# Optimization experiments

Measured on AMD Instinct MI355X. Metric: run time of the kernel, lower is better.

Reference implementation:

```python
import jax, jax.numpy as jnp
import numpy as np

D_MODEL = 2048
N_HEADS = 16
N_KV_HEADS = 4
D_HEAD = 128
MAX_SEQ_LEN = 4096
RANK = 32
GAMMA_INIT = 0.05
ROPE_BASE = 10000.0


def setup_inputs() -> dict:
    key = jax.random.key(0)
    ks = jax.random.split(key, 10)
    B, T = 1, 2048
    s = lambda fan_in: 1.0 / np.sqrt(fan_in)
    x = jax.random.normal(ks[0], (B, T, D_MODEL), dtype=jnp.float32)
    Wq = jax.random.normal(ks[1], (D_MODEL, N_HEADS * D_HEAD), dtype=jnp.float32) * s(D_MODEL)
    Wk = jax.random.normal(ks[2], (D_MODEL, N_KV_HEADS * D_HEAD), dtype=jnp.float32) * s(D_MODEL)
    Wv = jax.random.normal(ks[3], (D_MODEL, N_KV_HEADS * D_HEAD), dtype=jnp.float32) * s(D_MODEL)
    Wo = jax.random.normal(ks[4], (N_HEADS * D_HEAD, D_MODEL), dtype=jnp.float32) * s(N_HEADS * D_HEAD)
    pol_dir = jax.random.normal(ks[5], (N_HEADS,), dtype=jnp.float32) * 0.1
    pol_WA = jax.random.normal(ks[6], (D_MODEL, RANK), dtype=jnp.float32) * s(D_MODEL)
    pol_WB = jax.random.normal(ks[7], (D_MODEL, RANK), dtype=jnp.float32) * s(D_MODEL)
    pol_gate = jnp.full((N_HEADS,), -3.0, dtype=jnp.float32)
    # gtp_gamma initialized so softplus(gtp_gamma) == geometric ALiBi-style gamma schedule
    slopes = np.linspace(3.0, -3.0, N_HEADS)
    gamma_t = np.clip(GAMMA_INIT * 2.0 ** slopes, 1e-4, None)
    gtp_gamma = jnp.asarray(np.log(np.expm1(gamma_t)), dtype=jnp.float32)
    return {"x": x, "Wq": Wq, "Wk": Wk, "Wv": Wv, "Wo": Wo,
            "pol_dir": pol_dir, "pol_WA": pol_WA, "pol_WB": pol_WB,
            "pol_gate": pol_gate, "gtp_gamma": gtp_gamma}


def _rope(x, offset=0):
    # x: [B,H,T,D]; standard rotate-half RoPE
    B, H, T, D = x.shape
    inv_freq = 1.0 / (ROPE_BASE ** (jnp.arange(0, D, 2, dtype=jnp.float32) / D))
    pos = jnp.arange(T, dtype=jnp.float32) + offset
    ang = pos[:, None] * inv_freq[None, :]          # [T, D/2]
    cos = jnp.cos(ang)[None, None]                  # [1,1,T,D/2]
    sin = jnp.sin(ang)[None, None]
    x1, x2 = x[..., : D // 2], x[..., D // 2 :]
    return jnp.concatenate([x1 * cos - x2 * sin, x2 * cos + x1 * sin], axis=-1)


def reference(x, Wq, Wk, Wv, Wo, pol_dir, pol_WA, pol_WB, pol_gate, gtp_gamma):
    B, T, _ = x.shape
    H, Hkv, D = N_HEADS, N_KV_HEADS, D_HEAD
    n_rep = H // Hkv
    Q = (x @ Wq).reshape(B, T, H, D).transpose(0, 2, 1, 3)     # [B,H,T,D]
    K = (x @ Wk).reshape(B, T, Hkv, D).transpose(0, 2, 1, 3)   # [B,Hkv,T,D]
    V = (x @ Wv).reshape(B, T, Hkv, D).transpose(0, 2, 1, 3)
    Q = _rope(Q)
    K = _rope(K)
    K = jnp.repeat(K, n_rep, axis=1)                           # [B,H,T,D]
    V = jnp.repeat(V, n_rep, axis=1)

    # ---- attention bias ----
    idx = jnp.arange(T)
    delta = (idx[:, None] - idx[None, :]).astype(jnp.float32)  # [T,T], i - j
    causal = delta >= 0
    pol = jnp.clip(pol_dir, -1.0, 1.0)
    polarity_bias = -pol[:, None, None] * (delta / float(MAX_SEQ_LEN))[None]     # [H,T,T]
    gamma = jnp.maximum(jax.nn.softplus(gtp_gamma), 1e-6)
    gtp_bias = -gamma[:, None, None] * jnp.maximum(delta, 0.0)[None]             # [H,T,T]
    bias = (polarity_bias + gtp_bias)[None]                                      # [1,H,T,T]
    # low-rank content-dependent sigmoid bilinear term (prefill: q_len == k_len)
    A = x @ pol_WA                                                               # [B,T,r]
    Bm = x @ pol_WB                                                              # [B,T,r]
    M = jax.nn.sigmoid(jnp.einsum('bir,bjr->bij', A, Bm))                        # [B,T,T]
    gate = jax.nn.sigmoid(pol_gate)[None, :, None, None]
    bias = bias + gate * M[:, None]                                              # [B,H,T,T]
    neg_inf = jnp.finfo(bias.dtype).min
    bias = jnp.where(causal[None, None], bias, neg_inf)

    # ---- SDPA ----
    scores = jnp.einsum('bhid,bhjd->bhij', Q, K) / jnp.sqrt(jnp.float32(D)) + bias
    attn = jax.nn.softmax(scores, axis=-1)
    out = jnp.einsum('bhij,bhjd->bhid', attn, V)                                 # [B,H,T,D]
    out = out.transpose(0, 2, 1, 3).reshape(B, T, H * D)
    return out @ Wo
```

## Files before the change

### kernel.cpp

```cpp
#include <hip/hip_runtime.h>
#include <math.h>

typedef short bf16x8 __attribute__((ext_vector_type(8)));
typedef float f32x4  __attribute__((ext_vector_type(4)));

#define MFMA16 __builtin_amdgcn_mfma_f32_16x16x32_bf16
#define LOG2E 1.4426950408889634f

static __device__ __forceinline__ short f2bf(float f) {
  union { float f; unsigned u; } x; x.f = f;
  unsigned r = (x.u + 0x7FFFu + ((x.u >> 16) & 1u)) >> 16;
  return (short)r;
}
static __device__ __forceinline__ unsigned packbf(float a, float b) {
  return (unsigned)(unsigned short)f2bf(a) | ((unsigned)(unsigned short)f2bf(b) << 16);
}
static __device__ __forceinline__ float bf2f(short s) {
  union { unsigned u; float f; } x; x.u = ((unsigned)(unsigned short)s) << 16;
  return x.f;
}
static __device__ __forceinline__ void gload_lds16(const void* g, void* l) {
  __builtin_amdgcn_global_load_lds((const __attribute__((address_space(1))) void*)g,
                                   (__attribute__((address_space(3))) void*)l, 16, 0, 0);
}
static __device__ __forceinline__ float ex2(float x) {
  float r; asm("v_exp_f32 %0, %1" : "=v"(r) : "v"(x)); return r;
}
static __device__ __forceinline__ float rcpf(float x) {
  float r; asm("v_rcp_f32 %0, %1" : "=v"(r) : "v"(x)); return r;
}
static __device__ __forceinline__ unsigned cvtpk(float lo, float hi) {
  unsigned r; asm("v_cvt_pk_bf16_f32 %0, %1, %2" : "=v"(r) : "v"(lo), "v"(hi));
  return r;
}

__device__ __forceinline__ void tr_tile(
    const float* __restrict__ in, short* __restrict__ out,
    int K, int N, int nt, int kt, float (*t)[33])
{
  int n0 = nt * 32, k0 = kt * 32;
  int tx = threadIdx.x & 31, ty = threadIdx.x >> 5;
  #pragma unroll
  for (int i = 0; i < 4; ++i)
    t[ty + 8 * i][tx] = in[(size_t)(k0 + ty + 8 * i) * N + n0 + tx];
  __syncthreads();
  #pragma unroll
  for (int i = 0; i < 4; ++i)
    out[(size_t)(n0 + ty + 8 * i) * K + k0 + tx] = f2bf(t[tx][ty + 8 * i]);
}

__global__ __launch_bounds__(256) void prep_kernel(
    const float* __restrict__ x, const float* __restrict__ Wq,
    const float* __restrict__ Wk, const float* __restrict__ Wv,
    const float* __restrict__ WA, const float* __restrict__ WB,
    short* __restrict__ xb, short* __restrict__ Wqt, short* __restrict__ Wkt,
    short* __restrict__ Wvt, short* __restrict__ WABt)
{
  __shared__ float t[32][33];
  int b = blockIdx.x;
  if (b < 4096)       tr_tile(Wq, Wqt, 2048, 2048, b & 63, b >> 6, t);
  else if (b < 5120)  { int c = b - 4096; tr_tile(Wk, Wkt, 2048, 512, c & 15, c >> 4, t); }
  else if (b < 6144)  { int c = b - 5120; tr_tile(Wv, Wvt, 2048, 512, c & 15, c >> 4, t); }
  else if (b < 6208)  { int c = b - 6144; tr_tile(WA, WABt, 2048, 32, 0, c, t); }
  else if (b < 6272)  { int c = b - 6208; tr_tile(WB, WABt + 32 * 2048, 2048, 32, 0, c, t); }
  else {
    int i = (b - 6272) * 256 + threadIdx.x;
    float4 v = ((const float4*)x)[i];
    short4 o; o.x = f2bf(v.x); o.y = f2bf(v.y); o.z = f2bf(v.z); o.w = f2bf(v.w);
    ((short4*)xb)[i] = o;
  }
}

__global__ __launch_bounds__(256) void mid_kernel(
    const float* __restrict__ Wo, short* __restrict__ Wot,
    short* __restrict__ Q, short* __restrict__ K)
{
  __shared__ float t[32][33];
  int b = blockIdx.x;
  if (b < 4096) { tr_tile(Wo, Wot, 2048, 2048, b & 63, b >> 6, t); return; }
  int idx = (b - 4096) * 256 + threadIdx.x;
  int d  = idx & 63;
  int hh = (idx >> 6) % 20;
  int tt = idx / (20 * 64);
  short* base = (hh < 16) ? Q + (size_t)tt * 2048 + hh * 128 + d
                          : K + (size_t)tt * 512 + (hh - 16) * 128 + d;
  float inv = __expf((float)d * -0.14391156831212789f);
  float ang = (float)tt * inv;
  float sn, cs;
  __sincosf(ang, &sn, &cs);
  float x1 = bf2f(base[0]), x2 = bf2f(base[64]);
  base[0]  = f2bf(x1 * cs - x2 * sn);
  base[64] = f2bf(x2 * cs + x1 * sn);
}

__device__ __forceinline__ void gemm12864_core(
    const short* __restrict__ A, const short* __restrict__ Bt,
    int m0, int n0, int Kd, short* Asm , short* Bsm ,
    f32x4 acc[4][2])
{
  const int tid = threadIdx.x;
  const int lane = tid & 63, w = tid >> 6;
  const int lr = lane & 15, g4 = lane >> 4;
  const int wm = w >> 1, wn = w & 1;

  for (int k0 = 0; k0 < Kd; k0 += 64) {
    #pragma unroll
    for (int s = 0; s < 4; ++s) {
      int c = (s * 4 + w) * 64 + lane;
      int row = c >> 3, q = c & 7;
      gload_lds16(A + (size_t)(m0 + row) * Kd + k0 + (q ^ (row & 7)) * 8,
                  Asm + c * 8);
    }
    #pragma unroll
    for (int s = 0; s < 2; ++s) {
      int c = (s * 4 + w) * 64 + lane;
      int row = c >> 3, q = c & 7;
      gload_lds16(Bt + (size_t)(n0 + row) * Kd + k0 + (q ^ (row & 7)) * 8,
                  Bsm + c * 8);
    }
    __syncthreads();
    #pragma unroll
    for (int kk = 0; kk < 2; ++kk) {
      bf16x8 af[4], bff[2];
      #pragma unroll
      for (int mi = 0; mi < 4; ++mi) {
        int row = wm * 64 + mi * 16 + lr;
        af[mi] = *(const bf16x8*)(Asm + row * 64 +
                                  ((kk * 4 + g4) ^ (lr & 7)) * 8);
      }
      #pragma unroll
      for (int ni = 0; ni < 2; ++ni) {
        int row = wn * 32 + ni * 16 + lr;
        bff[ni] = *(const bf16x8*)(Bsm + row * 64 +
                                   ((kk * 4 + g4) ^ (lr & 7)) * 8);
      }
      #pragma unroll
      for (int mi = 0; mi < 4; ++mi)
        #pragma unroll
        for (int ni = 0; ni < 2; ++ni)
          acc[mi][ni] = MFMA16(af[mi], bff[ni], acc[mi][ni], 0, 0, 0);
    }
    __syncthreads();
  }
}

__global__ __launch_bounds__(256, 3) void gemm_qkv_kernel(
    const short* __restrict__ xb, const short* __restrict__ Wqt,
    const short* __restrict__ Wkt, const short* __restrict__ Wvt,
    const short* __restrict__ WABt,
    short* __restrict__ Qb, short* __restrict__ Kb, short* __restrict__ Vtb,
    short* __restrict__ Ab, short* __restrict__ Bb)
{
  __shared__ __align__(16) short Asm[128 * 64];
  __shared__ __align__(16) short Bsm[64 * 64];
  f32x4 acc[4][2];
  #pragma unroll
  for (int i = 0; i < 4; ++i)
    #pragma unroll
    for (int j = 0; j < 2; ++j) acc[i][j] = (f32x4){0.f, 0.f, 0.f, 0.f};

  const int bid = (int)blockIdx.x;
  const int swz = (bid & 7) * 98 + (bid >> 3);
  const int bx = swz % 49, by = swz / 49;

  const short* Bt; int mode, nl0;
  if (bx < 32)      { Bt = Wqt;  nl0 = bx * 64;        mode = 0; }
  else if (bx < 40) { Bt = Wkt;  nl0 = (bx - 32) * 64; mode = 1; }
  else if (bx < 48) { Bt = Wvt;  nl0 = (bx - 40) * 64; mode = 2; }
  else              { Bt = WABt; nl0 = 0;              mode = 3; }

  gemm12864_core(xb, Bt, by * 128, nl0, 2048, Asm, Bsm, acc);

  const int tid = threadIdx.x, lane = tid & 63, w = tid >> 6;
  const int lr = lane & 15, g4 = lane >> 4, wm = w >> 1, wn = w & 1;
  #pragma unroll
  for (int mi = 0; mi < 4; ++mi) {
    #pragma unroll
    for (int ni = 0; ni < 2; ++ni) {
      int mb = by * 128 + wm * 64 + mi * 16 + g4 * 4;
      int ncl = wn * 32 + ni * 16 + lr;
      int nc = nl0 + ncl;
      if (mode == 0) {
        #pragma unroll
        for (int r = 0; r < 4; ++r)
          Qb[(size_t)(mb + r) * 2048 + nc] = f2bf(acc[mi][ni][r]);
      } else if (mode == 1) {
        #pragma unroll
        for (int r = 0; r < 4; ++r)
          Kb[(size_t)(mb + r) * 512 + nc] = f2bf(acc[mi][ni][r]);
      } else if (mode == 2) {
        uint2 uu;
        uu.x = packbf(acc[mi][ni][0], acc[mi][ni][1]);
        uu.y = packbf(acc[mi][ni][2], acc[mi][ni][3]);
        *(uint2*)(Vtb + (size_t)nc * 2048 + mb) = uu;
      } else {
        #pragma unroll
        for (int r = 0; r < 4; ++r) {
          float sv = acc[mi][ni][r];
          if (ncl < 32) Ab[(size_t)(mb + r) * 32 + ncl] = f2bf(sv * LOG2E);
          else          Bb[(size_t)(mb + r) * 32 + (ncl - 32)] = f2bf(sv);
        }
      }
    }
  }
}

__global__ __launch_bounds__(256, 3) void gemm_out_kernel(
    const short* __restrict__ AO, const short* __restrict__ Wot,
    float* __restrict__ out)
{
  __shared__ __align__(16) short Asm[128 * 64];
  __shared__ __align__(16) short Bsm[64 * 64];
  f32x4 acc[4][2];
  #pragma unroll
  for (int i = 0; i < 4; ++i)
    #pragma unroll
    for (int j = 0; j < 2; ++j) acc[i][j] = (f32x4){0.f, 0.f, 0.f, 0.f};

  const int bid = (int)blockIdx.x;
  const int swz = (bid & 7) * 64 + (bid >> 3);
  const int bx = swz % 32, by = swz / 32;

  gemm12864_core(AO, Wot, by * 128, bx * 64, 2048, Asm, Bsm, acc);

  const int tid = threadIdx.x, lane = tid & 63, w = tid >> 6;
  const int lr = lane & 15, g4 = lane >> 4, wm = w >> 1, wn = w & 1;
  #pragma unroll
  for (int mi = 0; mi < 4; ++mi)
    #pragma unroll
    for (int ni = 0; ni < 2; ++ni) {
      int mb = by * 128 + wm * 64 + mi * 16 + g4 * 4;
      int nc = bx * 64 + wn * 32 + ni * 16 + lr;
      #pragma unroll
      for (int r = 0; r < 4; ++r)
        out[(size_t)(mb + r) * 2048 + nc] = acc[mi][ni][r];
    }
}

__global__ __launch_bounds__(256, 2) void attn_kernel(
    const short* __restrict__ Qg, const short* __restrict__ Kg,
    const short* __restrict__ Vtg, const short* __restrict__ Ag,
    const short* __restrict__ Bg, const float* __restrict__ pol_dir,
    const float* __restrict__ pol_gate, const float* __restrict__ gtp_gamma,
    short* __restrict__ AO)
{
  __shared__ __align__(16) char lds[73728];
  char* const K0s = lds;
  char* const K1s = lds + 16384;
  char* const V0s = lds + 32768;
  char* const V1s = lds + 49152;
  char* const Pb  = lds + 65536;

  const int tid = threadIdx.x;
  const int lane = tid & 63, w = tid >> 6;
  const int lr = lane & 15, g4 = lane >> 4;
  const int h  = blockIdx.x;
  const int by = blockIdx.y;
  const int qt = (by < 16) ? (31 - by) : (by - 16);
  const int q0 = qt * 64;
  const int kvh = h >> 2;
  const short* Kh = Kg + kvh * 128;
  const short* Vh = Vtg + (size_t)(kvh * 128) * 2048;

  float pol   = fminf(fmaxf(pol_dir[h], -1.f), 1.f);
  float gamma = fmaxf(log1pf(__expf(gtp_gamma[h])), 1e-6f);
  float gate  = (1.f / (1.f + __expf(-pol_gate[h]))) * LOG2E;
  const float c_h  = -(pol * (1.f / 4096.f) + gamma) * LOG2E;
  const float c16  = 16.f * c_h;
  const float chr1 = c_h, chr2 = c_h + c_h, chr3 = chr2 + c_h;
  const float sc = 0.08838834764831845f * LOG2E;
  const f32x4 z4 = {0.f, 0.f, 0.f, 0.f};

  #pragma unroll
  for (int s = 0; s < 4; ++s) {
    int idx = (w * 4 + s) * 64 + lane;
    int row = idx >> 4, slot = idx & 15;
    gload_lds16(Kh + (size_t)row * 512 + (slot ^ (row & 7)) * 8,
                K0s + (w * 4 + s) * 1024);
  }
  #pragma unroll
  for (int s = 0; s < 4; ++s) {
    int idx = (w * 4 + s) * 64 + lane;
    int row = idx >> 3, slot = idx & 7;
    gload_lds16(Vh + (size_t)row * 2048 + (slot ^ (row & 7)) * 8,
                V0s + (w * 4 + s) * 1024);
  }
  bf16x8 bA0, bA1, bA2, bA3, bB0, bB1, bB2, bB3;
  bA0 = *(const bf16x8*)(Bg + (size_t)(0 * 16 + lr) * 32 + g4 * 8);
  bA1 = *(const bf16x8*)(Bg + (size_t)(1 * 16 + lr) * 32 + g4 * 8);
  bA2 = *(const bf16x8*)(Bg + (size_t)(2 * 16 + lr) * 32 + g4 * 8);
  bA3 = *(const bf16x8*)(Bg + (size_t)(3 * 16 + lr) * 32 + g4 * 8);

  #pragma unroll
  for (int s = 0; s < 4; ++s) {
    int c = tid + s * 256;
    int row = c >> 4, sl = c & 15;
    int4 v = *(const int4*)(Qg + (size_t)(q0 + row) * 2048 + h * 128 + sl * 8);
    *(int4*)(K1s + row * 256 + ((sl * 16) ^ ((row & 7) << 4))) = v;
  }
  {
    int row = tid >> 2, sl = tid & 3;
    int4 va = *(const int4*)(Ag + (size_t)(q0 + row) * 32 + sl * 8);
    *(int4*)(Pb + row * 80 + sl * 16) = va;
  }
  asm volatile("s_waitcnt lgkmcnt(0)" ::: "memory");
  __builtin_amdgcn_s_barrier();

  bf16x8 qf[4];
  #pragma unroll
  for (int kk = 0; kk < 4; ++kk)
    qf[kk] = *(const bf16x8*)(K1s + (w * 16 + lr) * 256 +
                              ((kk * 64 + g4 * 16) ^ ((lr & 7) << 4)));
  bf16x8 afr = *(const bf16x8*)(Pb + (w * 16 + lr) * 80 + g4 * 16);
  asm volatile("s_waitcnt lgkmcnt(0)" ::: "memory");
  __builtin_amdgcn_s_barrier();

  f32x4 acc_o[8];
  #pragma unroll
  for (int i = 0; i < 8; ++i) acc_o[i] = z4;
  float m_st = -INFINITY, l_st = 0.f;
  char* const Pw = Pb + w * 2048;

#define ATTN_TILE(JT, KC, VC, KN, VN, BC0, BC1, BC2, BC3, BN0, BN1, BN2, BN3) \
  do {                                                                        \
    const int j0 = (JT) * 64;                                                 \
    const bool pf = (JT) < qt;                                                \
    if (pf) {                                                                 \
      _Pragma("unroll")                                                       \
      for (int s = 0; s < 4; ++s) {                                           \
        int idx = (w * 4 + s) * 64 + lane;                                    \
        int row = idx >> 4, slot = idx & 15;                                  \
        gload_lds16(Kh + (size_t)(j0 + 64 + row) * 512 + (slot ^ (row & 7)) * 8, \
                    (KN) + (w * 4 + s) * 1024);                               \
      }                                                                       \
      _Pragma("unroll")                                                       \
      for (int s = 0; s < 4; ++s) {                                           \
        int idx = (w * 4 + s) * 64 + lane;                                    \
        int row = idx >> 3, slot = idx & 7;                                   \
        gload_lds16(Vh + (size_t)row * 2048 + (j0 + 64) + (slot ^ (row & 7)) * 8, \
                    (VN) + (w * 4 + s) * 1024);                               \
      }                                                                       \
      BN0 = *(const bf16x8*)(Bg + (size_t)(j0 + 64 + 0 * 16 + lr) * 32 + g4 * 8); \
      BN1 = *(const bf16x8*)(Bg + (size_t)(j0 + 64 + 1 * 16 + lr) * 32 + g4 * 8); \
      BN2 = *(const bf16x8*)(Bg + (size_t)(j0 + 64 + 2 * 16 + lr) * 32 + g4 * 8); \
      BN3 = *(const bf16x8*)(Bg + (size_t)(j0 + 64 + 3 * 16 + lr) * 32 + g4 * 8); \
      asm volatile("s_waitcnt vmcnt(12)" ::: "memory");                       \
    } else {                                                                  \
      asm volatile("s_waitcnt vmcnt(0)" ::: "memory");                        \
    }                                                                         \
    __builtin_amdgcn_s_barrier();         \
    f32x4 acc_s[4], md4[4];                                                   \
    __builtin_amdgcn_s_setprio(1);                                            \
    _Pragma("unroll")                                                         \
    for (int cb = 0; cb < 4; ++cb) {                                          \
      acc_s[cb] = z4;                                                         \
      _Pragma("unroll")                                                       \
      for (int kk = 0; kk < 4; ++kk) {                                        \
        bf16x8 kf = *(const bf16x8*)((KC) + (cb * 16 + lr) * 256 +            \
                                     ((kk * 64 + g4 * 16) ^ ((lr & 7) << 4)));\
        acc_s[cb] = MFMA16(kf, qf[kk], acc_s[cb], 0, 0, 0);                   \
      }                                                                       \
    }                                                                         \
    md4[0] = MFMA16(BC0, afr, z4, 0, 0, 0);                                   \
    md4[1] = MFMA16(BC1, afr, z4, 0, 0, 0);                                   \
    md4[2] = MFMA16(BC2, afr, z4, 0, 0, 0);                                   \
    md4[3] = MFMA16(BC3, afr, z4, 0, 0, 0);                                   \
    __builtin_amdgcn_s_setprio(0);                                            \
    const int dq = q0 + w * 16 + lr - j0;                                     \
    float bq = c_h * (float)(dq - g4 * 4);                                    \
    _Pragma("unroll")                                                         \
    for (int cb = 0; cb < 4; ++cb) {                                          \
      float bcb = bq - c16 * (float)cb;                                       \
      float sig0 = rcpf(1.f + ex2(-md4[cb][0]));                              \
      float sig1 = rcpf(1.f + ex2(-md4[cb][1]));                              \
      float sig2 = rcpf(1.f + ex2(-md4[cb][2]));                              \
      float sig3 = rcpf(1.f + ex2(-md4[cb][3]));                              \
      acc_s[cb][0] = fmaf(acc_s[cb][0], sc, fmaf(gate, sig0, bcb));           \
      acc_s[cb][1] = fmaf(acc_s[cb][1], sc, fmaf(gate, sig1, bcb - chr1));    \
      acc_s[cb][2] = fmaf(acc_s[cb][2], sc, fmaf(gate, sig2, bcb - chr2));    \
      acc_s[cb][3] = fmaf(acc_s[cb][3], sc, fmaf(gate, sig3, bcb - chr3));    \
    }                                                                         \
    if ((JT) == qt) {                                                         \
      _Pragma("unroll")                                                       \
      for (int cb = 0; cb < 4; ++cb)                                          \
        _Pragma("unroll")                                                     \
        for (int r = 0; r < 4; ++r)                                           \
          if (cb * 16 + g4 * 4 + r > dq) acc_s[cb][r] = -INFINITY;            \
    }                                                                         \
    float t0 = fmaxf(fmaxf(acc_s[0][0], acc_s[0][1]), acc_s[0][2]);           \
    float t1 = fmaxf(fmaxf(acc_s[0][3], acc_s[1][0]), acc_s[1][1]);           \
    float t2 = fmaxf(fmaxf(acc_s[1][2], acc_s[1][3]), acc_s[2][0]);           \
    float t3 = fmaxf(fmaxf(acc_s[2][1], acc_s[2][2]), acc_s[2][3]);           \
    float t4 = fmaxf(fmaxf(acc_s[3][0], acc_s[3][1]), acc_s[3][2]);           \
    float mx = fmaxf(fmaxf(fmaxf(t0, t1), t2),                                \
                     fmaxf(fmaxf(t3, t4), acc_s[3][3]));                      \
    mx = fmaxf(mx, __shfl_xor(mx, 16));                                       \
    mx = fmaxf(mx, __shfl_xor(mx, 32));                                       \
    if (!__all(mx - m_st <= 11.5415603f)) {                                   \
      float mn = fmaxf(m_st, mx);                                             \
      float es = ex2(m_st - mn);                                              \
      l_st *= es;                                                             \
      m_st = mn;                                                              \
      float es4[4];                                                           \
      _Pragma("unroll")                                                       \
      for (int r = 0; r < 4; ++r) es4[r] = __shfl(es, g4 * 4 + r, 64);        \
      _Pragma("unroll")                                                       \
      for (int db = 0; db < 8; ++db)                                          \
        _Pragma("unroll")                                                     \
        for (int r = 0; r < 4; ++r) acc_o[db][r] *= es4[r];                   \
    }                                                                         \
    float rs = 0.f;                                                           \
    _Pragma("unroll")                                                         \
    for (int cb = 0; cb < 4; ++cb)                                            \
      _Pragma("unroll")                                                       \
      for (int r = 0; r < 4; ++r) {                                           \
        float p = ex2(acc_s[cb][r] - m_st);                                   \
        acc_s[cb][r] = p;                                                     \
        rs += p;                                                              \
      }                                                                       \
    rs += __shfl_xor(rs, 16);                                                 \
    rs += __shfl_xor(rs, 32);                                                 \
    l_st += rs;                                                               \
    _Pragma("unroll")                                                         \
    for (int cb = 0; cb < 4; ++cb) {                                          \
      uint2 uu;                                                               \
      uu.x = cvtpk(acc_s[cb][0], acc_s[cb][1]);                               \
      uu.y = cvtpk(acc_s[cb][2], acc_s[cb][3]);                               \
      *(uint2*)(Pw + lr * 128 + ((cb * 32 + g4 * 8) ^ ((lr & 7) << 4))) = uu; \
    }                                                                         \
    asm volatile("s_waitcnt lgkmcnt(0)" ::: "memory");                        \
    __builtin_amdgcn_sched_barrier(0);                                        \
    __builtin_amdgcn_s_setprio(1);                                            \
    _Pragma("unroll")                                                         \
    for (int kk = 0; kk < 2; ++kk) {                                          \
      bf16x8 pfr = *(const bf16x8*)(Pw + lr * 128 +                           \
                                    ((kk * 64 + g4 * 16) ^ ((lr & 7) << 4))); \
      _Pragma("unroll")                                                       \
      for (int db = 0; db < 8; ++db) {                                        \
        bf16x8 vf = *(const bf16x8*)((VC) + (db * 16 + lr) * 128 +            \
                                     ((kk * 64 + g4 * 16) ^ ((lr & 7) << 4)));\
        acc_o[db] = MFMA16(pfr, vf, acc_o[db], 0, 0, 0);                      \
      }                                                                       \
    }                                                                         \
    __builtin_amdgcn_s_setprio(0);                                            \
    asm volatile("s_waitcnt lgkmcnt(0)" ::: "memory");                        \
    __builtin_amdgcn_s_barrier();           \
  } while (0)

  for (int jt = 0; jt <= qt; jt += 2) {
    ATTN_TILE(jt, K0s, V0s, K1s, V1s, bA0, bA1, bA2, bA3, bB0, bB1, bB2, bB3);
    if (jt + 1 <= qt)
      ATTN_TILE(jt + 1, K1s, V1s, K0s, V0s, bB0, bB1, bB2, bB3,
                bA0, bA1, bA2, bA3);
  }
#undef ATTN_TILE

  float lrcp[4];
  #pragma unroll
  for (int r = 0; r < 4; ++r) lrcp[r] = 1.f / __shfl(l_st, g4 * 4 + r, 64);
  #pragma unroll
  for (int db = 0; db < 8; ++db)
    #pragma unroll
    for (int r = 0; r < 4; ++r)
      AO[(size_t)(q0 + w * 16 + g4 * 4 + r) * 2048 + h * 128 + db * 16 + lr] =
          f2bf(acc_o[db][r] * lrcp[r]);
}

extern "C" void kernel_launch(void* const* d_in, const int* in_sizes, int n_in,
                              void* d_out, int out_size, void* d_ws, size_t ws_size,
                              hipStream_t stream) {
  const float* x         = (const float*)d_in[0];
  const float* Wq        = (const float*)d_in[1];
  const float* Wk        = (const float*)d_in[2];
  const float* Wv        = (const float*)d_in[3];
  const float* Wo        = (const float*)d_in[4];
  const float* pol_dir   = (const float*)d_in[5];
  const float* pol_WA    = (const float*)d_in[6];
  const float* pol_WB    = (const float*)d_in[7];
  const float* pol_gate  = (const float*)d_in[8];
  const float* gtp_gamma = (const float*)d_in[9];
  float* out = (float*)d_out;

  char* ws = (char*)d_ws;
  short* Qb   = (short*)(ws);
  short* Kb   = (short*)(ws + 8388608);
  short* Vtb  = (short*)(ws + 10485760);
  short* Ab   = (short*)(ws + 12582912);
  short* Bb   = (short*)(ws + 12713984);
  short* xb   = (short*)(ws + 12845056);
  short* Wot  = xb;
  short* Wqt  = (short*)(ws + 21233664);
  short* AO   = Wqt;
  short* Wkt  = (short*)(ws + 29622272);
  short* Wvt  = (short*)(ws + 31719424);
  short* WABt = (short*)(ws + 33816576);

  prep_kernel<<<10368, 256, 0, stream>>>(x, Wq, Wk, Wv, pol_WA, pol_WB,
                                         xb, Wqt, Wkt, Wvt, WABt);
  gemm_qkv_kernel<<<784, 256, 0, stream>>>(xb, Wqt, Wkt, Wvt, WABt,
                                           Qb, Kb, Vtb, Ab, Bb);
  mid_kernel<<<14336, 256, 0, stream>>>(Wo, Wot, Qb, Kb);
  attn_kernel<<<dim3(16, 32), 256, 0, stream>>>(Qb, Kb, Vtb, Ab, Bb,
                                                pol_dir, pol_gate, gtp_gamma, AO);
  gemm_out_kernel<<<512, 256, 0, stream>>>(AO, Wot, out);
}
```

Baseline: 156.9 us.

## Split long causal query tiles across two blocks and fold RoPE into attention

Query tiles 16-31 are each split into two KV ranges handled by separate blocks. The blocks write unnormalized bf16 partial outputs plus max/sum stats, and a new combine kernel merges them, which evens out the causal load imbalance. RoPE for Q is now applied inside the attention kernel from a precomputed cos/sin table, and only K gets a small standalone RoPE kernel. The Wo transpose moves into the prep kernel, and attention drops to a single V buffer (49KB LDS instead of 72KB) with the V and B-factor prefetch rescheduled. The costs are an extra launch, extra partial-output traffic, and bf16 rounding of the partials before the combine.

```diff
diff --git a/kernel.cpp b/kernel.cpp
--- a/kernel.cpp
+++ b/kernel.cpp
@@ -53,8 +53,10 @@
     const float* __restrict__ x, const float* __restrict__ Wq,
     const float* __restrict__ Wk, const float* __restrict__ Wv,
     const float* __restrict__ WA, const float* __restrict__ WB,
+    const float* __restrict__ Wo,
     short* __restrict__ xb, short* __restrict__ Wqt, short* __restrict__ Wkt,
-    short* __restrict__ Wvt, short* __restrict__ WABt)
+    short* __restrict__ Wvt, short* __restrict__ WABt, short* __restrict__ Wot,
+    float* __restrict__ RTab)
 {
   __shared__ float t[32][33];
   int b = blockIdx.x;
@@ -63,31 +65,36 @@
   else if (b < 6144)  { int c = b - 5120; tr_tile(Wv, Wvt, 2048, 512, c & 15, c >> 4, t); }
   else if (b < 6208)  { int c = b - 6144; tr_tile(WA, WABt, 2048, 32, 0, c, t); }
   else if (b < 6272)  { int c = b - 6208; tr_tile(WB, WABt + 32 * 2048, 2048, 32, 0, c, t); }
-  else {
+  else if (b < 10368) {
     int i = (b - 6272) * 256 + threadIdx.x;
     float4 v = ((const float4*)x)[i];
     short4 o; o.x = f2bf(v.x); o.y = f2bf(v.y); o.z = f2bf(v.z); o.w = f2bf(v.w);
     ((short4*)xb)[i] = o;
-  }
-}
-
-__global__ __launch_bounds__(256) void mid_kernel(
-    const float* __restrict__ Wo, short* __restrict__ Wot,
-    short* __restrict__ Q, short* __restrict__ K)
-{
-  __shared__ float t[32][33];
-  int b = blockIdx.x;
-  if (b < 4096) { tr_tile(Wo, Wot, 2048, 2048, b & 63, b >> 6, t); return; }
-  int idx = (b - 4096) * 256 + threadIdx.x;
+  } else if (b < 14464) {
+    int c = b - 10368;
+    tr_tile(Wo, Wot, 2048, 2048, c & 63, c >> 6, t);
+  } else {
+    int i = (b - 14464) * 256 + threadIdx.x;
+    int d = i & 63, tt = i >> 6;
+    float inv = __expf((float)d * -0.14391156831212789f);
+    float ang = (float)tt * inv;
+    float sn, cs;
+    __sincosf(ang, &sn, &cs);
+    RTab[(size_t)i * 2]     = cs;
+    RTab[(size_t)i * 2 + 1] = sn;
+  }
+}
+
+__global__ __launch_bounds__(256) void ropek_kernel(short* __restrict__ K,
+                                                    const float* __restrict__ RTab)
+{
+  int idx = blockIdx.x * 256 + threadIdx.x;
   int d  = idx & 63;
-  int hh = (idx >> 6) % 20;
-  int tt = idx / (20 * 64);
-  short* base = (hh < 16) ? Q + (size_t)tt * 2048 + hh * 128 + d
-                          : K + (size_t)tt * 512 + (hh - 16) * 128 + d;
-  float inv = __expf((float)d * -0.14391156831212789f);
-  float ang = (float)tt * inv;
-  float sn, cs;
-  __sincosf(ang, &sn, &cs);
+  int hh = (idx >> 6) & 3;
+  int tt = idx >> 8;
+  short* base = K + (size_t)tt * 512 + hh * 128 + d;
+  float cs = RTab[((size_t)tt * 64 + d) * 2];
+  float sn = RTab[((size_t)tt * 64 + d) * 2 + 1];
   float x1 = bf2f(base[0]), x2 = bf2f(base[64]);
   base[0]  = f2bf(x1 * cs - x2 * sn);
   base[64] = f2bf(x2 * cs + x1 * sn);
@@ -242,21 +249,23 @@
     const short* __restrict__ Vtg, const short* __restrict__ Ag,
     const short* __restrict__ Bg, const float* __restrict__ pol_dir,
     const float* __restrict__ pol_gate, const float* __restrict__ gtp_gamma,
-    short* __restrict__ AO)
-{
-  __shared__ __align__(16) char lds[73728];
+    const float* __restrict__ RTab, short* __restrict__ AO,
+    short* __restrict__ Opart, float* __restrict__ MLp)
+{
+  __shared__ __align__(16) char lds[49152];
   char* const K0s = lds;
   char* const K1s = lds + 16384;
-  char* const V0s = lds + 32768;
-  char* const V1s = lds + 49152;
-  char* const Pb  = lds + 65536;
+  char* const Vs  = lds + 32768;
 
   const int tid = threadIdx.x;
   const int lane = tid & 63, w = tid >> 6;
   const int lr = lane & 15, g4 = lane >> 4;
   const int h  = blockIdx.x;
-  const int by = blockIdx.y;
-  const int qt = (by < 16) ? (31 - by) : (by - 16);
+  const int y  = blockIdx.y;
+  int qt, jlo, jhi, half;
+  if (y < 16)      { qt = 16 + y; int c1 = (qt + 2) >> 1; jlo = 0;  jhi = c1 - 1; half = 0; }
+  else if (y < 32) { qt = y;      int c1 = (qt + 2) >> 1; jlo = c1; jhi = qt;     half = 1; }
+  else             { qt = 47 - y; jlo = 0; jhi = qt; half = -1; }
   const int q0 = qt * 64;
   const int kvh = h >> 2;
   const short* Kh = Kg + kvh * 128;
@@ -275,56 +284,75 @@
   for (int s = 0; s < 4; ++s) {
     int idx = (w * 4 + s) * 64 + lane;
     int row = idx >> 4, slot = idx & 15;
-    gload_lds16(Kh + (size_t)row * 512 + (slot ^ (row & 7)) * 8,
+    gload_lds16(Kh + (size_t)(jlo * 64 + row) * 512 + (slot ^ (row & 7)) * 8,
                 K0s + (w * 4 + s) * 1024);
   }
+  bf16x8 bA0, bA1, bA2, bA3, bB0, bB1, bB2, bB3;
+  bA0 = *(const bf16x8*)(Bg + (size_t)(jlo * 64 + 0 * 16 + lr) * 32 + g4 * 8);
+  bA1 = *(const bf16x8*)(Bg + (size_t)(jlo * 64 + 1 * 16 + lr) * 32 + g4 * 8);
+  bA2 = *(const bf16x8*)(Bg + (size_t)(jlo * 64 + 2 * 16 + lr) * 32 + g4 * 8);
+  bA3 = *(const bf16x8*)(Bg + (size_t)(jlo * 64 + 3 * 16 + lr) * 32 + g4 * 8);
+
+  #pragma unroll
+  for (int s = 0; s < 2; ++s) {
+    int c = tid + s * 256;
+    int row = c >> 3, sl = c & 7;
+    const short* qrow = Qg + (size_t)(q0 + row) * 2048 + h * 128;
+    int4 vlo = *(const int4*)(qrow + sl * 8);
+    int4 vhi = *(const int4*)(qrow + 64 + sl * 8);
+    const float* tabrow = RTab + (size_t)(q0 + row) * 128 + sl * 16;
+    float tab[16];
+    *(float4*)(tab + 0)  = *(const float4*)(tabrow + 0);
+    *(float4*)(tab + 4)  = *(const float4*)(tabrow + 4);
+    *(float4*)(tab + 8)  = *(const float4*)(tabrow + 8);
+    *(float4*)(tab + 12) = *(const float4*)(tabrow + 12);
+    short* lop = (short*)&vlo;
+    short* hip = (short*)&vhi;
+    short rlo[8], rhi[8];
+    #pragma unroll
+    for (int j = 0; j < 8; ++j) {
+      float cs = tab[2 * j], sn = tab[2 * j + 1];
+      float x1 = bf2f(lop[j]), x2 = bf2f(hip[j]);
+      rlo[j] = f2bf(x1 * cs - x2 * sn);
+      rhi[j] = f2bf(x2 * cs + x1 * sn);
+    }
+    *(int4*)(K1s + row * 256 + ((sl * 16) ^ ((row & 7) << 4))) = *(int4*)rlo;
+    *(int4*)(K1s + row * 256 + (((sl + 8) * 16) ^ ((row & 7) << 4))) = *(int4*)rhi;
+  }
+  {
+    int row = tid >> 2, sl = tid & 3;
+    int4 va = *(const int4*)(Ag + (size_t)(q0 + row) * 32 + sl * 8);
+    *(int4*)(Vs + row * 80 + sl * 16) = va;
+  }
+  asm volatile("s_waitcnt lgkmcnt(0)" ::: "memory");
+  __builtin_amdgcn_s_barrier();
+
+  bf16x8 qf[4];
+  #pragma unroll
+  for (int kk = 0; kk < 4; ++kk)
+    qf[kk] = *(const bf16x8*)(K1s + (w * 16 + lr) * 256 +
+                              ((kk * 64 + g4 * 16) ^ ((lr & 7) << 4)));
+  bf16x8 afr = *(const bf16x8*)(Vs + (w * 16 + lr) * 80 + g4 * 16);
+  asm volatile("s_waitcnt lgkmcnt(0)" ::: "memory");
+  __builtin_amdgcn_s_barrier();
+
   #pragma unroll
   for (int s = 0; s < 4; ++s) {
     int idx = (w * 4 + s) * 64 + lane;
     int row = idx >> 3, slot = idx & 7;
-    gload_lds16(Vh + (size_t)row * 2048 + (slot ^ (row & 7)) * 8,
-                V0s + (w * 4 + s) * 1024);
-  }
-  bf16x8 bA0, bA1, bA2, bA3, bB0, bB1, bB2, bB3;
-  bA0 = *(const bf16x8*)(Bg + (size_t)(0 * 16 + lr) * 32 + g4 * 8);
-  bA1 = *(const bf16x8*)(Bg + (size_t)(1 * 16 + lr) * 32 + g4 * 8);
-  bA2 = *(const bf16x8*)(Bg + (size_t)(2 * 16 + lr) * 32 + g4 * 8);
-  bA3 = *(const bf16x8*)(Bg + (size_t)(3 * 16 + lr) * 32 + g4 * 8);
-
-  #pragma unroll
-  for (int s = 0; s < 4; ++s) {
-    int c = tid + s * 256;
-    int row = c >> 4, sl = c & 15;
-    int4 v = *(const int4*)(Qg + (size_t)(q0 + row) * 2048 + h * 128 + sl * 8);
-    *(int4*)(K1s + row * 256 + ((sl * 16) ^ ((row & 7) << 4))) = v;
-  }
-  {
-    int row = tid >> 2, sl = tid & 3;
-    int4 va = *(const int4*)(Ag + (size_t)(q0 + row) * 32 + sl * 8);
-    *(int4*)(Pb + row * 80 + sl * 16) = va;
-  }
-  asm volatile("s_waitcnt lgkmcnt(0)" ::: "memory");
-  __builtin_amdgcn_s_barrier();
-
-  bf16x8 qf[4];
-  #pragma unroll
-  for (int kk = 0; kk < 4; ++kk)
-    qf[kk] = *(const bf16x8*)(K1s + (w * 16 + lr) * 256 +
-                              ((kk * 64 + g4 * 16) ^ ((lr & 7) << 4)));
-  bf16x8 afr = *(const bf16x8*)(Pb + (w * 16 + lr) * 80 + g4 * 16);
-  asm volatile("s_waitcnt lgkmcnt(0)" ::: "memory");
-  __builtin_amdgcn_s_barrier();
+    gload_lds16(Vh + (size_t)row * 2048 + jlo * 64 + (slot ^ (row & 7)) * 8,
+                Vs + (w * 4 + s) * 1024);
+  }
 
   f32x4 acc_o[8];
   #pragma unroll
   for (int i = 0; i < 8; ++i) acc_o[i] = z4;
   float m_st = -INFINITY, l_st = 0.f;
-  char* const Pw = Pb + w * 2048;
-
-#define ATTN_TILE(JT, KC, VC, KN, VN, BC0, BC1, BC2, BC3, BN0, BN1, BN2, BN3) \
+
+#define ATTN_TILE(JT, KC, KN, BC0, BC1, BC2, BC3, BN0, BN1, BN2, BN3)         \
   do {                                                                        \
     const int j0 = (JT) * 64;                                                 \
-    const bool pf = (JT) < qt;                                                \
+    const bool pf = (JT) < jhi;                                               \
     if (pf) {                                                                 \
       _Pragma("unroll")                                                       \
       for (int s = 0; s < 4; ++s) {                                           \
@@ -333,22 +361,11 @@
         gload_lds16(Kh + (size_t)(j0 + 64 + row) * 512 + (slot ^ (row & 7)) * 8, \
                     (KN) + (w * 4 + s) * 1024);                               \
       }                                                                       \
-      _Pragma("unroll")                                                       \
-      for (int s = 0; s < 4; ++s) {                                           \
-        int idx = (w * 4 + s) * 64 + lane;                                    \
-        int row = idx >> 3, slot = idx & 7;                                   \
-        gload_lds16(Vh + (size_t)row * 2048 + (j0 + 64) + (slot ^ (row & 7)) * 8, \
-                    (VN) + (w * 4 + s) * 1024);                               \
-      }                                                                       \
-      BN0 = *(const bf16x8*)(Bg + (size_t)(j0 + 64 + 0 * 16 + lr) * 32 + g4 * 8); \
-      BN1 = *(const bf16x8*)(Bg + (size_t)(j0 + 64 + 1 * 16 + lr) * 32 + g4 * 8); \
-      BN2 = *(const bf16x8*)(Bg + (size_t)(j0 + 64 + 2 * 16 + lr) * 32 + g4 * 8); \
-      BN3 = *(const bf16x8*)(Bg + (size_t)(j0 + 64 + 3 * 16 + lr) * 32 + g4 * 8); \
-      asm volatile("s_waitcnt vmcnt(12)" ::: "memory");                       \
+      asm volatile("s_waitcnt vmcnt(8)" ::: "memory");                        \
     } else {                                                                  \
-      asm volatile("s_waitcnt vmcnt(0)" ::: "memory");                        \
-    }                                                                         \
-    __builtin_amdgcn_s_barrier();         \
+      asm volatile("s_waitcnt vmcnt(4)" ::: "memory");                        \
+    }                                                                         \
+    __builtin_amdgcn_s_barrier();                \
     f32x4 acc_s[4], md4[4];                                                   \
     __builtin_amdgcn_s_setprio(1);                                            \
     _Pragma("unroll")                                                         \
@@ -366,6 +383,12 @@
     md4[2] = MFMA16(BC2, afr, z4, 0, 0, 0);                                   \
     md4[3] = MFMA16(BC3, afr, z4, 0, 0, 0);                                   \
     __builtin_amdgcn_s_setprio(0);                                            \
+    if (pf) {                                                                 \
+      BN0 = *(const bf16x8*)(Bg + (size_t)(j0 + 64 + 0 * 16 + lr) * 32 + g4 * 8); \
+      BN1 = *(const bf16x8*)(Bg + (size_t)(j0 + 64 + 1 * 16 + lr) * 32 + g4 * 8); \
+      BN2 = *(const bf16x8*)(Bg + (size_t)(j0 + 64 + 2 * 16 + lr) * 32 + g4 * 8); \
+      BN3 = *(const bf16x8*)(Bg + (size_t)(j0 + 64 + 3 * 16 + lr) * 32 + g4 * 8); \
+    }                                                                         \
     const int dq = q0 + w * 16 + lr - j0;                                     \
     float bq = c_h * (float)(dq - g4 * 4);                                    \
     _Pragma("unroll")                                                         \
@@ -421,6 +444,10 @@
     rs += __shfl_xor(rs, 16);                                                 \
     rs += __shfl_xor(rs, 32);                                                 \
     l_st += rs;                                                               \
+    if (pf) asm volatile("s_waitcnt vmcnt(8)" ::: "memory");                  \
+    else    asm volatile("s_waitcnt vmcnt(0)" ::: "memory");                  \
+    __builtin_amdgcn_s_barrier();           \
+    char* Pw = (KC) + w * 2048;                                               \
     _Pragma("unroll")                                                         \
     for (int cb = 0; cb < 4; ++cb) {                                          \
       uint2 uu;                                                               \
@@ -437,33 +464,85 @@
                                     ((kk * 64 + g4 * 16) ^ ((lr & 7) << 4))); \
       _Pragma("unroll")                                                       \
       for (int db = 0; db < 8; ++db) {                                        \
-        bf16x8 vf = *(const bf16x8*)((VC) + (db * 16 + lr) * 128 +            \
+        bf16x8 vf = *(const bf16x8*)(Vs + (db * 16 + lr) * 128 +              \
                                      ((kk * 64 + g4 * 16) ^ ((lr & 7) << 4)));\
         acc_o[db] = MFMA16(pfr, vf, acc_o[db], 0, 0, 0);                      \
       }                                                                       \
     }                                                                         \
     __builtin_amdgcn_s_setprio(0);                                            \
     asm volatile("s_waitcnt lgkmcnt(0)" ::: "memory");                        \
-    __builtin_amdgcn_s_barrier();           \
+    __builtin_amdgcn_sched_barrier(0);                                        \
+    __builtin_amdgcn_s_barrier();                         \
+    if (pf) {                                                                 \
+      _Pragma("unroll")                                                       \
+      for (int s = 0; s < 4; ++s) {                                           \
+        int idx = (w * 4 + s) * 64 + lane;                                    \
+        int row = idx >> 3, slot = idx & 7;                                   \
+        gload_lds16(Vh + (size_t)row * 2048 + (j0 + 64) + (slot ^ (row & 7)) * 8, \
+                    Vs + (w * 4 + s) * 1024);                                 \
+      }                                                                       \
+    }                                                                         \
   } while (0)
 
-  for (int jt = 0; jt <= qt; jt += 2) {
-    ATTN_TILE(jt, K0s, V0s, K1s, V1s, bA0, bA1, bA2, bA3, bB0, bB1, bB2, bB3);
-    if (jt + 1 <= qt)
-      ATTN_TILE(jt + 1, K1s, V1s, K0s, V0s, bB0, bB1, bB2, bB3,
-                bA0, bA1, bA2, bA3);
+  for (int jt = jlo; jt <= jhi; jt += 2) {
+    ATTN_TILE(jt, K0s, K1s, bA0, bA1, bA2, bA3, bB0, bB1, bB2, bB3);
+    if (jt + 1 <= jhi)
+      ATTN_TILE(jt + 1, K1s, K0s, bB0, bB1, bB2, bB3, bA0, bA1, bA2, bA3);
   }
 #undef ATTN_TILE
 
-  float lrcp[4];
-  #pragma unroll
-  for (int r = 0; r < 4; ++r) lrcp[r] = 1.f / __shfl(l_st, g4 * 4 + r, 64);
-  #pragma unroll
-  for (int db = 0; db < 8; ++db)
-    #pragma unroll
-    for (int r = 0; r < 4; ++r)
-      AO[(size_t)(q0 + w * 16 + g4 * 4 + r) * 2048 + h * 128 + db * 16 + lr] =
-          f2bf(acc_o[db][r] * lrcp[r]);
+  if (half < 0) {
+    float lrcp[4];
+    #pragma unroll
+    for (int r = 0; r < 4; ++r) lrcp[r] = 1.f / __shfl(l_st, g4 * 4 + r, 64);
+    #pragma unroll
+    for (int db = 0; db < 8; ++db)
+      #pragma unroll
+      for (int r = 0; r < 4; ++r)
+        AO[(size_t)(q0 + w * 16 + g4 * 4 + r) * 2048 + h * 128 + db * 16 + lr] =
+            f2bf(acc_o[db][r] * lrcp[r]);
+  } else {
+    short* Op = Opart + ((size_t)half * 16 + h) * (1024 * 128);
+    int rowb = q0 - 1024 + w * 16;
+    #pragma unroll
+    for (int db = 0; db < 8; ++db)
+      #pragma unroll
+      for (int r = 0; r < 4; ++r)
+        Op[(size_t)(rowb + g4 * 4 + r) * 128 + db * 16 + lr] = f2bf(acc_o[db][r]);
+    if (g4 == 0) {
+      size_t mi = (((size_t)half * 16 + h) * 1024 + (size_t)(rowb + lr)) * 2;
+      MLp[mi]     = m_st;
+      MLp[mi + 1] = l_st;
+    }
+  }
+}
+
+__global__ __launch_bounds__(256) void combine_kernel(
+    const short* __restrict__ Opart, const float* __restrict__ MLp,
+    short* __restrict__ AO)
+{
+  int idx = blockIdx.x * 256 + threadIdx.x;
+  int ch = idx & 15;
+  int rl = (idx >> 4) & 1023;
+  int h  = idx >> 14;
+  size_t r0 = ((size_t)h * 1024 + rl) * 2;
+  float m0 = MLp[r0],               l0 = MLp[r0 + 1];
+  float m1 = MLp[16 * 1024 * 2 + r0], l1 = MLp[16 * 1024 * 2 + r0 + 1];
+  float M  = fmaxf(m0, m1);
+  float w0 = ex2(m0 - M), w1 = ex2(m1 - M);
+  float rden = rcpf(fmaf(l0, w0, l1 * w1));
+  float f0 = w0 * rden, f1 = w1 * rden;
+  const short* O0 = Opart + (size_t)h * (1024 * 128) + (size_t)rl * 128 + ch * 8;
+  const short* O1 = O0 + (size_t)16 * 1024 * 128;
+  int4 a = *(const int4*)O0;
+  int4 b = *(const int4*)O1;
+  const short* ap = (const short*)&a;
+  const short* bp = (const short*)&b;
+  short o[8];
+  #pragma unroll
+  for (int j = 0; j < 8; ++j)
+    o[j] = f2bf(bf2f(ap[j]) * f0 + bf2f(bp[j]) * f1);
+  *(int4*)(AO + (size_t)(1024 + rl) * 2048 + h * 128 + ch * 8) = *(int4*)o;
 }
 
 extern "C" void kernel_launch(void* const* d_in, const int* in_sizes, int n_in,
@@ -487,20 +566,25 @@
   short* Vtb  = (short*)(ws + 10485760);
   short* Ab   = (short*)(ws + 12582912);
   short* Bb   = (short*)(ws + 12713984);
-  short* xb   = (short*)(ws + 12845056);
-  short* Wot  = xb;
+  short* Wot  = (short*)(ws + 12845056);
   short* Wqt  = (short*)(ws + 21233664);
   short* AO   = Wqt;
   short* Wkt  = (short*)(ws + 29622272);
   short* Wvt  = (short*)(ws + 31719424);
   short* WABt = (short*)(ws + 33816576);
-
-  prep_kernel<<<10368, 256, 0, stream>>>(x, Wq, Wk, Wv, pol_WA, pol_WB,
-                                         xb, Wqt, Wkt, Wvt, WABt);
+  short* xb   = (short*)(ws + 34340864);
+  short* Opart = xb;
+  float* RTab = (float*)(ws + 42729472);
+  float* MLp  = (float*)(ws + 43778048);
+
+  prep_kernel<<<14976, 256, 0, stream>>>(x, Wq, Wk, Wv, pol_WA, pol_WB, Wo,
+                                         xb, Wqt, Wkt, Wvt, WABt, Wot, RTab);
   gemm_qkv_kernel<<<784, 256, 0, stream>>>(xb, Wqt, Wkt, Wvt, WABt,
                                            Qb, Kb, Vtb, Ab, Bb);
-  mid_kernel<<<14336, 256, 0, stream>>>(Wo, Wot, Qb, Kb);
-  attn_kernel<<<dim3(16, 32), 256, 0, stream>>>(Qb, Kb, Vtb, Ab, Bb,
-                                                pol_dir, pol_gate, gtp_gamma, AO);
+  ropek_kernel<<<2048, 256, 0, stream>>>(Kb, RTab);
+  attn_kernel<<<dim3(16, 48), 256, 0, stream>>>(Qb, Kb, Vtb, Ab, Bb,
+                                                pol_dir, pol_gate, gtp_gamma,
+                                                RTab, AO, Opart, MLp);
+  combine_kernel<<<1024, 256, 0, stream>>>(Opart, MLp, AO);
   gemm_out_kernel<<<512, 256, 0, stream>>>(AO, Wot, out);
 }
```

After: 156.7 us. Within noise of the previous version (-0.1%).
